# Performance work log

Measured on AMD Instinct MI355X. Metric: run time of the kernel, lower is better.

Reference implementation:

```python
import jax, jax.numpy as jnp
import numpy as np

D_MODEL = 512

def setup_inputs() -> dict:
    key = jax.random.key(0)
    ks = jax.random.split(key, 8)
    B, SQ, SKV, D = 4, 2048, 4096, D_MODEL
    scale = 1.0 / np.sqrt(D)
    return {
        "x": jax.random.normal(ks[0], (B, SQ, D), dtype=jnp.float32),
        "encoder_out": jax.random.normal(ks[1], (B, SKV, D), dtype=jnp.float32),
        "wq": jax.random.normal(ks[2], (D, D), dtype=jnp.float32) * scale,
        "bq": jax.random.normal(ks[3], (D,), dtype=jnp.float32) * 0.01,
        "wk": jax.random.normal(ks[4], (D, D), dtype=jnp.float32) * scale,
        "bk": jax.random.normal(ks[5], (D,), dtype=jnp.float32) * 0.01,
        "wv": jax.random.normal(ks[6], (D, D), dtype=jnp.float32) * scale,
        "bv": jax.random.normal(ks[7], (D,), dtype=jnp.float32) * 0.01,
    }

def reference(x, encoder_out, wq, bq, wk, bk, wv, bv):
    # torch Linear: y = x @ W.T + b
    q = jnp.einsum('bsd,ed->bse', x, wq) + bq            # [B,Sq,D]
    k = jnp.einsum('btd,ed->bte', encoder_out, wk) + bk  # [B,Skv,D]
    v = jnp.einsum('btd,ed->bte', encoder_out, wv) + bv  # [B,Skv,D]
    d_k = q.shape[-1]
    scores = jnp.einsum('bse,bte->bst', q, k) / jnp.sqrt(jnp.asarray(d_k, q.dtype))
    weights = jax.nn.softmax(scores, axis=-1)            # [B,Sq,Skv]
    return jnp.einsum('bst,bte->bse', weights, v)        # [B,Sq,D]
```

## Files before the change

kernel.cpp:

```cpp
#include <hip/hip_runtime.h>
#include <hip/hip_bf16.h>


typedef __bf16 bf16;
typedef __attribute__((ext_vector_type(8))) __bf16 bf16x8;
typedef __attribute__((ext_vector_type(4))) float f32x4;

#define DM 512

__device__ __forceinline__ void gload_lds16(const bf16* g, bf16* l)
{
    __builtin_amdgcn_global_load_lds(
        (const __attribute__((address_space(1))) void*)g,
        (__attribute__((address_space(3))) void*)l, 16, 0, 0);
}

__global__ __launch_bounds__(256) void cvt_all_kernel(
    const float* __restrict__ x,   bf16* __restrict__ xb,
    const float* __restrict__ enc, bf16* __restrict__ encb,
    const float* __restrict__ wq,  bf16* __restrict__ wqb,
    const float* __restrict__ wk,  bf16* __restrict__ wkb,
    const float* __restrict__ wv,  bf16* __restrict__ wvb)
{
    int g = blockIdx.x * 256 + threadIdx.x;
    const float* src; bf16* dst;
    if (g < 524288)       { src = x;   dst = xb; }
    else if (g < 1572864) { g -= 524288;  src = enc; dst = encb; }
    else if (g < 1605632) { g -= 1572864; src = wq;  dst = wqb; }
    else if (g < 1638400) { g -= 1605632; src = wk;  dst = wkb; }
    else                  { g -= 1638400; src = wv;  dst = wvb; }
    const float4 f0 = *reinterpret_cast<const float4*>(src + (size_t)g * 8);
    const float4 f1 = *reinterpret_cast<const float4*>(src + (size_t)g * 8 + 4);
    bf16x8 v;
    v[0]=(bf16)f0.x; v[1]=(bf16)f0.y; v[2]=(bf16)f0.z; v[3]=(bf16)f0.w;
    v[4]=(bf16)f1.x; v[5]=(bf16)f1.y; v[6]=(bf16)f1.z; v[7]=(bf16)f1.w;
    *reinterpret_cast<bf16x8*>(dst + (size_t)g * 8) = v;
}

template<bool KV>
__global__ __launch_bounds__(256) void proj_kernel(const bf16* __restrict__ A,
    const bf16* __restrict__ W0, const float* __restrict__ b0, bf16* __restrict__ out0,
    const bf16* __restrict__ W1, const float* __restrict__ b1, bf16* __restrict__ out1)
{
    __shared__ __align__(16) bf16 As[2][64][40];
    __shared__ __align__(16) bf16 W0s[2][64][40];
    __shared__ __align__(16) bf16 W1s[2][64][40];

    const int tid  = threadIdx.x;
    const int w    = tid >> 6, lane = tid & 63, quad = lane >> 4, l15 = lane & 15;
    const int wr   = w >> 1, wc = w & 1;
    const int n0   = blockIdx.x * 64;
    const int m0   = blockIdx.y * 64;
    const int srow = tid >> 2;
    const int scol = (tid & 3) * 8;

    f32x4 acc0[2][2] = {}, acc1[2][2] = {};
    bf16x8 ra, rw0, rw1;

    auto prefetch = [&](int kk) {
        ra  = *reinterpret_cast<const bf16x8*>(A  + (size_t)(m0 + srow) * DM + kk + scol);
        rw0 = *reinterpret_cast<const bf16x8*>(W0 + (size_t)(n0 + srow) * DM + kk + scol);
        if constexpr (KV)
            rw1 = *reinterpret_cast<const bf16x8*>(W1 + (size_t)(n0 + srow) * DM + kk + scol);
    };
    auto store_lds = [&](int p) {
        *reinterpret_cast<bf16x8*>(&As[p][srow][scol])  = ra;
        *reinterpret_cast<bf16x8*>(&W0s[p][srow][scol]) = rw0;
        if constexpr (KV)
            *reinterpret_cast<bf16x8*>(&W1s[p][srow][scol]) = rw1;
    };

    prefetch(0);
    store_lds(0);
    __syncthreads();

    for (int step = 0; step < 16; step++) {
        const int p = step & 1;
        if (step < 15) prefetch((step + 1) * 32);

        bf16x8 af[2], bf0[2], bf1[2];
#pragma unroll
        for (int mt = 0; mt < 2; mt++)
            af[mt] = *reinterpret_cast<const bf16x8*>(&As[p][32*wr + 16*mt + l15][quad*8]);
#pragma unroll
        for (int nt = 0; nt < 2; nt++)
            bf0[nt] = *reinterpret_cast<const bf16x8*>(&W0s[p][32*wc + 16*nt + l15][quad*8]);
        if constexpr (KV) {
#pragma unroll
            for (int nt = 0; nt < 2; nt++)
                bf1[nt] = *reinterpret_cast<const bf16x8*>(&W1s[p][32*wc + 16*nt + l15][quad*8]);
        }
#pragma unroll
        for (int mt = 0; mt < 2; mt++)
#pragma unroll
            for (int nt = 0; nt < 2; nt++) {
                acc0[mt][nt] = __builtin_amdgcn_mfma_f32_16x16x32_bf16(af[mt], bf0[nt], acc0[mt][nt], 0, 0, 0);
                if constexpr (KV)
                    acc1[mt][nt] = __builtin_amdgcn_mfma_f32_16x16x32_bf16(af[mt], bf1[nt], acc1[mt][nt], 0, 0, 0);
            }

        if (step < 15) store_lds(p ^ 1);
        __syncthreads();
    }

#pragma unroll
    for (int mt = 0; mt < 2; mt++)
#pragma unroll
        for (int nt = 0; nt < 2; nt++) {
            const int coll = 32*wc + 16*nt + l15;
            const int rowl = 32*wr + 16*mt + quad*4;
            {
                const float bv = b0[n0 + coll];
                f32x4 c = acc0[mt][nt];
#pragma unroll
                for (int r = 0; r < 4; r++)
                    out0[(size_t)(m0 + rowl + r) * DM + n0 + coll] = (bf16)(c[r] + bv);
            }
            if constexpr (KV) {
                const float bv = b1[n0 + coll];
                f32x4 c = acc1[mt][nt];
                const int gr = m0 + rowl;
                const int bidx = gr >> 12, t = gr & 4095;
                const int e = n0 + coll;
                union { uint2 u; bf16 h[4]; } pk;
#pragma unroll
                for (int r = 0; r < 4; r++) pk.h[r] = (bf16)(c[r] + bv);
                *reinterpret_cast<uint2*>(out1 +
                    ((((size_t)(bidx*128 + (t >> 5)) * DM + e) << 5) + (t & 31))) = pk.u;
            }
        }
}

__global__ __launch_bounds__(512, 2) void attn_kernel(const bf16* __restrict__ Qb,
                                                      const bf16* __restrict__ Kb,
                                                      const bf16* __restrict__ Vtg,
                                                      float* __restrict__ Op,
                                                      float* __restrict__ lp)
{
    __shared__ __align__(16) bf16 Kt[2][64][512];
    __shared__ __align__(16) bf16 Ps[64][80];
    __shared__ float lred[64];

    const int tid  = threadIdx.x;
    const int w    = tid >> 6, lane = tid & 63, quad = lane >> 4, l15 = lane & 15;
    const int qb   = w >> 1;
    const int cb0  = (w & 1) * 2;

    const int id = blockIdx.x;
    const int combo = id & 7, qblk = id >> 3;
    const int b = combo & 3, z = combo >> 2;
    const int q0 = qblk * 64;
    const int NT = 32, tb = z * 2048;

    bf16x8 af[16];
    {
        const bf16* qsrc = Qb + (size_t)(b*2048 + q0 + 16*qb + l15) * DM + quad*8;
#pragma unroll
        for (int k4 = 0; k4 < 16; k4++) af[k4] = *reinterpret_cast<const bf16x8*>(qsrc + k4*32);
    }
    if (tid < 64) lred[tid] = 0.f;

    const bf16* kbase = Kb + (size_t)(b*4096 + tb) * DM;
#pragma unroll
    for (int i = 0; i < 8; i++) {
        const int row = w + 8*i;
        gload_lds16(kbase + (size_t)row * DM + ((lane ^ w) * 8), &Kt[0][row][0]);
    }
    __syncthreads();

    f32x4 oacc[4][4] = {};
    float lsum[2][4] = {};
    const float kexp = 1.44269504088896f * 0.044194173824159216f;
    const int sxor = (l15 & 7) << 4;

    for (int t = 0; t < NT; t++) {
        const int buf = t & 1;

        if (t + 1 < NT) {
            const bf16* ksrc = kbase + (size_t)(t + 1) * 64 * DM;
#pragma unroll
            for (int i = 0; i < 8; i++) {
                const int row = w + 8*i;
                gload_lds16(ksrc + (size_t)row * DM + ((lane ^ w) * 8), &Kt[buf ^ 1][row][0]);
            }
        }

        bf16x8 vf[4][2];
#pragma unroll
        for (int ks = 0; ks < 2; ks++) {
            const size_t tblk = (size_t)(b*128 + z*64 + t*2 + ks) * DM;
#pragma unroll
            for (int nt = 0; nt < 4; nt++)
                vf[nt][ks] = *reinterpret_cast<const bf16x8*>(
                    Vtg + ((tblk + 64*w + 16*nt + l15) << 5) + quad*8);
        }

        f32x4 sacc[2] = {};
        const char* krowA = (const char*)&Kt[buf][16*cb0 + l15][0];
        const char* krowB = (const char*)&Kt[buf][16*cb0 + 16 + l15][0];
#pragma unroll
        for (int k4 = 0; k4 < 16; k4++) {
            const int off = (k4*64 + quad*16) ^ sxor;
            bf16x8 k0 = *reinterpret_cast<const bf16x8*>(krowA + off);
            bf16x8 k1 = *reinterpret_cast<const bf16x8*>(krowB + off);
            sacc[0] = __builtin_amdgcn_mfma_f32_16x16x32_bf16(af[k4], k0, sacc[0], 0, 0, 0);
            sacc[1] = __builtin_amdgcn_mfma_f32_16x16x32_bf16(af[k4], k1, sacc[1], 0, 0, 0);
        }

#pragma unroll
        for (int s = 0; s < 2; s++)
#pragma unroll
            for (int r = 0; r < 4; r++) {
                const float p = exp2f(sacc[s][r] * kexp);
                lsum[s][r] += p;
                Ps[16*qb + quad*4 + r][16*(cb0 + s) + l15] = (bf16)p;
            }
        __syncthreads();

#pragma unroll
        for (int ks = 0; ks < 2; ks++) {
            bf16x8 ap[4];
#pragma unroll
            for (int mt = 0; mt < 4; mt++)
                ap[mt] = *reinterpret_cast<const bf16x8*>(&Ps[16*mt + l15][ks*32 + quad*8]);
#pragma unroll
            for (int nt = 0; nt < 4; nt++)
#pragma unroll
                for (int mt = 0; mt < 4; mt++)
                    oacc[mt][nt] = __builtin_amdgcn_mfma_f32_16x16x32_bf16(ap[mt], vf[nt][ks], oacc[mt][nt], 0, 0, 0);
        }
        __syncthreads();
    }

#pragma unroll
    for (int r = 0; r < 4; r++)
        atomicAdd(&lred[16*qb + quad*4 + r], lsum[0][r] + lsum[1][r]);
    __syncthreads();

    if (tid < 64) lp[(size_t)z * 8192 + b * 2048 + q0 + tid] = lred[tid];
#pragma unroll
    for (int mt = 0; mt < 4; mt++)
#pragma unroll
        for (int r = 0; r < 4; r++) {
            const int row = 16*mt + quad*4 + r;
            float* obase = Op + ((size_t)z * 8192 + b * 2048 + q0 + row) * DM;
#pragma unroll
            for (int nt = 0; nt < 4; nt++)
                obase[64*w + 16*nt + l15] = oacc[mt][nt][r];
        }
}

__global__ __launch_bounds__(256) void reduce_kernel(const float* __restrict__ Op,
                                                     const float* __restrict__ lp,
                                                     float* __restrict__ out)
{
    const int g = blockIdx.x * 256 + threadIdx.x;
    const size_t e = (size_t)g * 4;
    const int row = g >> 7;
    float4 o = *reinterpret_cast<const float4*>(Op + e);
    float4 a = *reinterpret_cast<const float4*>(Op + 4194304 + e);
    const float l = lp[row] + lp[8192 + row];
    const float linv = 1.0f / l;
    o.x = (o.x + a.x) * linv;
    o.y = (o.y + a.y) * linv;
    o.z = (o.z + a.z) * linv;
    o.w = (o.w + a.w) * linv;
    *reinterpret_cast<float4*>(out + e) = o;
}

extern "C" void kernel_launch(void* const* d_in, const int* in_sizes, int n_in,
                              void* d_out, int out_size, void* d_ws, size_t ws_size,
                              hipStream_t stream)
{
    const float* x   = (const float*)d_in[0];
    const float* enc = (const float*)d_in[1];
    const float* wq  = (const float*)d_in[2];
    const float* bq  = (const float*)d_in[3];
    const float* wk  = (const float*)d_in[4];
    const float* bk  = (const float*)d_in[5];
    const float* wv  = (const float*)d_in[6];
    const float* bv  = (const float*)d_in[7];
    float* out = (float*)d_out;

    char* ws = (char*)d_ws;
    bf16*  Qb   = (bf16*)ws;
    bf16*  Kb   = (bf16*)(ws + 8388608);
    bf16*  Vtg  = (bf16*)(ws + 25165824);
    bf16*  xb   = (bf16*)(ws + 41943040);
    bf16*  encb = (bf16*)(ws + 50331648);
    bf16*  wqb  = (bf16*)(ws + 67108864);
    bf16*  wkb  = (bf16*)(ws + 67633152);
    bf16*  wvb  = (bf16*)(ws + 68157440);
    float* Op   = (float*)(ws + 41943040);
    float* lp   = (float*)(ws + 41943040 + 2ull * 16777216);

    hipLaunchKernelGGL(cvt_all_kernel, dim3(6528), dim3(256), 0, stream,
                       x, xb, enc, encb, wq, wqb, wk, wkb, wv, wvb);

    hipLaunchKernelGGL((proj_kernel<false>), dim3(8, 128), dim3(256), 0, stream,
                       xb, wqb, bq, Qb, (const bf16*)nullptr, (const float*)nullptr, (bf16*)nullptr);
    hipLaunchKernelGGL((proj_kernel<true>),  dim3(8, 256), dim3(256), 0, stream,
                       encb, wkb, bk, Kb, wvb, bv, Vtg);

    hipLaunchKernelGGL(attn_kernel, dim3(256), dim3(512), 0, stream, Qb, Kb, Vtg, Op, lp);
    hipLaunchKernelGGL(reduce_kernel, dim3(4096), dim3(256), 0, stream, Op, lp, out);
}
```

Baseline: 270.1 us.

## Remap QK^T wave tiling to share K fragments and widen LDS swizzle

Each wave now covers 32 query rows by 16 key columns instead of 16 rows by 32 columns. One K fragment read from LDS is reused across two Q fragments, halving K LDS reads per wave at the cost of doubling Q registers held in af. The K tile swizzle is widened from an 8-way to a 16-way XOR, and the next-tile K prefetch is issued after the V global loads. The mid-loop __syncthreads is replaced by an explicit lgkmcnt wait, s_barrier and sched_barrier. The extra Q registers raise register pressure under the 512x2 launch bounds and risk spilling.

```diff
diff --git a/kernel.cpp b/kernel.cpp
--- a/kernel.cpp
+++ b/kernel.cpp
@@ -143,8 +143,8 @@
 
     const int tid  = threadIdx.x;
     const int w    = tid >> 6, lane = tid & 63, quad = lane >> 4, l15 = lane & 15;
-    const int qb   = w >> 1;
-    const int cb0  = (w & 1) * 2;
+    const int qh   = w >> 2;
+    const int cw   = w & 3;
 
     const int id = blockIdx.x;
     const int combo = id & 7, qblk = id >> 3;
@@ -152,11 +152,13 @@
     const int q0 = qblk * 64;
     const int NT = 32, tb = z * 2048;
 
-    bf16x8 af[16];
-    {
-        const bf16* qsrc = Qb + (size_t)(b*2048 + q0 + 16*qb + l15) * DM + quad*8;
-#pragma unroll
-        for (int k4 = 0; k4 < 16; k4++) af[k4] = *reinterpret_cast<const bf16x8*>(qsrc + k4*32);
+    bf16x8 af[2][16];
+#pragma unroll
+    for (int mt = 0; mt < 2; mt++) {
+        const bf16* qsrc = Qb + (size_t)(b*2048 + q0 + 32*qh + 16*mt + l15) * DM + quad*8;
+#pragma unroll
+        for (int k4 = 0; k4 < 16; k4++)
+            af[mt][k4] = *reinterpret_cast<const bf16x8*>(qsrc + k4*32);
     }
     if (tid < 64) lred[tid] = 0.f;
 
@@ -164,26 +166,17 @@
 #pragma unroll
     for (int i = 0; i < 8; i++) {
         const int row = w + 8*i;
-        gload_lds16(kbase + (size_t)row * DM + ((lane ^ w) * 8), &Kt[0][row][0]);
+        gload_lds16(kbase + (size_t)row * DM + ((lane ^ (row & 15)) * 8), &Kt[0][row][0]);
     }
     __syncthreads();
 
     f32x4 oacc[4][4] = {};
     float lsum[2][4] = {};
     const float kexp = 1.44269504088896f * 0.044194173824159216f;
-    const int sxor = (l15 & 7) << 4;
+    const int sxor = l15 << 4;
 
     for (int t = 0; t < NT; t++) {
         const int buf = t & 1;
-
-        if (t + 1 < NT) {
-            const bf16* ksrc = kbase + (size_t)(t + 1) * 64 * DM;
-#pragma unroll
-            for (int i = 0; i < 8; i++) {
-                const int row = w + 8*i;
-                gload_lds16(ksrc + (size_t)row * DM + ((lane ^ w) * 8), &Kt[buf ^ 1][row][0]);
-            }
-        }
 
         bf16x8 vf[4][2];
 #pragma unroll
@@ -195,27 +188,37 @@
                     Vtg + ((tblk + 64*w + 16*nt + l15) << 5) + quad*8);
         }
 
+        if (t + 1 < NT) {
+            const bf16* ksrc = kbase + (size_t)(t + 1) * 64 * DM;
+#pragma unroll
+            for (int i = 0; i < 8; i++) {
+                const int row = w + 8*i;
+                gload_lds16(ksrc + (size_t)row * DM + ((lane ^ (row & 15)) * 8), &Kt[buf ^ 1][row][0]);
+            }
+        }
+
         f32x4 sacc[2] = {};
-        const char* krowA = (const char*)&Kt[buf][16*cb0 + l15][0];
-        const char* krowB = (const char*)&Kt[buf][16*cb0 + 16 + l15][0];
+        const char* krow = (const char*)&Kt[buf][16*cw + l15][0];
 #pragma unroll
         for (int k4 = 0; k4 < 16; k4++) {
             const int off = (k4*64 + quad*16) ^ sxor;
-            bf16x8 k0 = *reinterpret_cast<const bf16x8*>(krowA + off);
-            bf16x8 k1 = *reinterpret_cast<const bf16x8*>(krowB + off);
-            sacc[0] = __builtin_amdgcn_mfma_f32_16x16x32_bf16(af[k4], k0, sacc[0], 0, 0, 0);
-            sacc[1] = __builtin_amdgcn_mfma_f32_16x16x32_bf16(af[k4], k1, sacc[1], 0, 0, 0);
-        }
-
-#pragma unroll
-        for (int s = 0; s < 2; s++)
+            bf16x8 kf = *reinterpret_cast<const bf16x8*>(krow + off);
+            sacc[0] = __builtin_amdgcn_mfma_f32_16x16x32_bf16(af[0][k4], kf, sacc[0], 0, 0, 0);
+            sacc[1] = __builtin_amdgcn_mfma_f32_16x16x32_bf16(af[1][k4], kf, sacc[1], 0, 0, 0);
+        }
+
+#pragma unroll
+        for (int mt = 0; mt < 2; mt++)
 #pragma unroll
             for (int r = 0; r < 4; r++) {
-                const float p = exp2f(sacc[s][r] * kexp);
-                lsum[s][r] += p;
-                Ps[16*qb + quad*4 + r][16*(cb0 + s) + l15] = (bf16)p;
-            }
-        __syncthreads();
+                const float p = exp2f(sacc[mt][r] * kexp);
+                lsum[mt][r] += p;
+                Ps[32*qh + 16*mt + quad*4 + r][16*cw + l15] = (bf16)p;
+            }
+
+        asm volatile("s_waitcnt lgkmcnt(0)" ::: "memory");
+        __builtin_amdgcn_s_barrier();
+        __builtin_amdgcn_sched_barrier(0);
 
 #pragma unroll
         for (int ks = 0; ks < 2; ks++) {
@@ -233,8 +236,10 @@
     }
 
 #pragma unroll
-    for (int r = 0; r < 4; r++)
-        atomicAdd(&lred[16*qb + quad*4 + r], lsum[0][r] + lsum[1][r]);
+    for (int mt = 0; mt < 2; mt++)
+#pragma unroll
+        for (int r = 0; r < 4; r++)
+            atomicAdd(&lred[32*qh + 16*mt + quad*4 + r], lsum[mt][r]);
     __syncthreads();
 
     if (tid < 64) lp[(size_t)z * 8192 + b * 2048 + q0 + tid] = lred[tid];
```

New measurement: 352.9 us. 1.31x slower.
